# Kernel tuning notes

Measured on AMD Instinct MI355X. Metric: run time of the kernel, lower is better.

The kernel has to match this reference:

```python
import jax, jax.numpy as jnp
import numpy as np

N = 500_000
K = 16
E = N * K
H = 256


def _linear_params(key, fan_in, fan_out):
    k1, k2 = jax.random.split(key)
    bound = 1.0 / np.sqrt(fan_in)
    W = jax.random.uniform(k1, (fan_in, fan_out), jnp.float32, -bound, bound)
    b = jax.random.uniform(k2, (fan_out,), jnp.float32, -bound, bound)
    return W, b


def setup_inputs() -> dict:
    key = jax.random.key(0)
    ks = jax.random.split(key, 10)
    x = jax.random.normal(ks[0], (N, 3), jnp.float32)
    edge_index = jax.random.randint(ks[1], (2, E), 0, N, jnp.int64)
    edge_attr = jax.random.normal(ks[2], (E, 1), jnp.float32)
    W1, b1 = _linear_params(ks[3], K, H)          # GNN1 message MLP: Linear(k, 256)
    We1, be1 = _linear_params(ks[4], H, 128)      # encoder Linear(256,128)
    We2, be2 = _linear_params(ks[5], 128, 6)      # encoder Linear(128,6)
    Wd1, bd1 = _linear_params(ks[6], 6, 128)      # decoder Linear(6,128)
    Wd2, bd2 = _linear_params(ks[7], 128, H)      # decoder Linear(128,256)
    Wo, bo = _linear_params(ks[8], H, 1)          # output Linear(256,1)
    return {"x": x, "edge_index": edge_index, "edge_attr": edge_attr,
            "W1": W1, "b1": b1, "We1": We1, "be1": be1, "We2": We2, "be2": be2,
            "Wd1": Wd1, "bd1": bd1, "Wd2": Wd2, "bd2": bd2, "Wo": Wo, "bo": bo}


def reference(x, edge_index, edge_attr, W1, b1, We1, be1, We2, be2,
              Wd1, bd1, Wd2, bd2, Wo, bo):
    # GNN1: messages are edge_attr verbatim (x_i/x_j ignored); aggregate reshapes
    # all E scalar messages into (N, k) (k edges per node, contiguous) and runs
    # Linear(k,256)+Tanh. Note: LSTM and GCN4 branches in the torch code are dead
    # (GNN1 ignores its node-feature input), so they do not affect the output.
    k = W1.shape[0]
    msgs = edge_attr.reshape(-1, k)                    # (N, k)
    h = jnp.tanh(msgs @ W1 + b1)                       # (N, 256)
    # second L1 call produces the identical result (depends only on edge_attr)
    z = jnp.tanh(jnp.tanh(h @ We1 + be1) @ We2 + be2)  # encoder -> (N, 6)
    d = jnp.tanh(z @ Wd1 + bd1) @ Wd2 + bd2            # decoder -> (N, 256)
    out = jax.nn.sigmoid(jnp.tanh(d) @ Wo + bo)        # (N, 1)
    return out[:, 0]                                   # squeeze(dim=1) -> (N,)
```

## Files before the change

kernel.cpp:

```cpp
#include <hip/hip_runtime.h>


#define N_NODES 500000

#define OFF_W1 0
#define OFF_W2 8192
#define OFF_W3 73728
#define OFF_W4 77824
#define OFF_W5 86016
#define OFF_WO 151552
#define OFF_B1 152576
#define OFF_B2 153600
#define OFF_B3 154112
#define OFF_B4 154176
#define OFF_B5 154688
#define OFF_EXTRA 155712
#define OFF_ZERO  155728
#define IMG_END   156240
#define IMG_ALLOC 156672

#define LDS_SZ IMG_ALLOC

#define SCONST (-2.8853900817779268f)

typedef _Float16 half8  __attribute__((ext_vector_type(8)));
typedef __fp16   pk16x2 __attribute__((ext_vector_type(2)));
typedef float    f32x4  __attribute__((ext_vector_type(4)));
typedef int      int4v  __attribute__((ext_vector_type(4)));

__device__ __align__(16) char g_img[IMG_ALLOC];

static __device__ __forceinline__ unsigned pack_f16_rne(float a, float b) {
  _Float16 ha = (_Float16)a, hb = (_Float16)b;
  unsigned short ua = __builtin_bit_cast(unsigned short, ha);
  unsigned short ub = __builtin_bit_cast(unsigned short, hb);
  return (unsigned)ua | ((unsigned)ub << 16);
}
static __device__ __forceinline__ int pkrtz(float a, float b) {
  pk16x2 h = __builtin_amdgcn_cvt_pkrtz(a, b);
  return __builtin_bit_cast(int, h);
}
static __device__ __forceinline__ float sig2(float y) {
  float e = __builtin_amdgcn_exp2f(y);
  return __builtin_amdgcn_rcpf(1.0f + e);
}
static __device__ __forceinline__ float sigmoid_f(float x) {
  float e = __builtin_amdgcn_exp2f(x * -1.4426950408889634f);
  return __builtin_amdgcn_rcpf(1.0f + e);
}
static __device__ __forceinline__ f32x4 mfma16(half8 a, int4v b, f32x4 c) {
  return __builtin_amdgcn_mfma_f32_16x16x32_f16(a, __builtin_bit_cast(half8, b), c, 0, 0, 0);
}
static __device__ __forceinline__ half8 lda(const char* smem, int off) {
  return *(const half8*)(smem + off);
}
static __device__ __forceinline__ f32x4 ldf4(const char* smem, int off) {
  return *(const f32x4*)(smem + off);
}
#define FENCE() __builtin_amdgcn_sched_barrier(0)

struct PK2 { int lo, hi; };
static __device__ __forceinline__ PK2 tp(f32x4 a) {
  PK2 p;
  p.lo = pkrtz(sig2(a.x), sig2(a.y));
  p.hi = pkrtz(sig2(a.z), sig2(a.w));
  return p;
}

__global__ __launch_bounds__(256)
void gnn_prep(const float* __restrict__ W1,  const float* __restrict__ b1,
              const float* __restrict__ We1, const float* __restrict__ be1,
              const float* __restrict__ We2, const float* __restrict__ be2,
              const float* __restrict__ Wd1, const float* __restrict__ bd1,
              const float* __restrict__ Wd2, const float* __restrict__ bd2,
              const float* __restrict__ Wo,  const float* __restrict__ bo)
{
  __shared__ float sb[832];
  const int tid = threadIdx.x;
  const int bx = blockIdx.x;

  if (bx >= 153) {
    float* gB2 = (float*)(g_img + OFF_B2);
    float* gB3 = (float*)(g_img + OFF_B3);
    float* gB4 = (float*)(g_img + OFF_B4);
    float* gB5 = (float*)(g_img + OFF_B5);
    if (bx == 153) {
      int col = tid & 127, part = tid >> 7;
      float s = 0.0f;
      for (int r = 0; r < 128; ++r) s += We1[(part * 128 + r) * 128 + col];
      sb[tid] = s;
      __syncthreads();
      if (tid < 128) gB2[tid] = SCONST * (be1[tid] - (sb[tid] + sb[128 + tid]));
    } else if (bx == 154) {
      float s = 0.0f;
      for (int r = 0; r < 128; ++r) s += Wd2[r * 256 + tid];
      gB5[tid] = SCONST * (bd2[tid] - s);
    } else {
      for (int j = tid; j < 768; j += 256) sb[j] = We2[j];
      if (tid >= 192) {
        int i = tid - 192;
        sb[768 + i] = Wo[4 * i] + Wo[4 * i + 1] + Wo[4 * i + 2] + Wo[4 * i + 3];
      }
      __syncthreads();
      if (tid < 6) {
        float s = 0.0f;
        for (int k = 0; k < 128; ++k) s += sb[k * 6 + tid];
        gB3[tid] = SCONST * (be2[tid] - s);
      } else if (tid < 16) {
        gB3[tid] = 0.0f;
      } else if (tid == 16) {
        float s = 0.0f;
        for (int i = 0; i < 64; ++i) s += sb[768 + i];
        *(float*)(g_img + OFF_EXTRA) = bo[0] - s;
      } else if (tid >= 32 && tid < 160) {
        int i = tid - 32;
        float s = 0.0f;
        for (int k = 0; k < 6; ++k) s += Wd1[k * 128 + i];
        gB4[i] = SCONST * (bd1[i] - s);
      }
    }
    return;
  }

  int off = (bx * 256 + tid) * 4;
  if (off >= IMG_END) return;
  if (off >= OFF_B2 && off < OFF_EXTRA + 4) return;
  unsigned val;
  if (off < OFF_W2) {
    int rel = off;
    int mi = rel >> 9, li = (rel >> 4) & 31, j2 = (rel >> 2) & 3;
    int fout = mi * 16 + (li & 15);
    int k0 = (li >> 4) * 8 + j2 * 2;
    val = pack_f16_rne(SCONST * W1[k0 * 256 + fout], SCONST * W1[(k0 + 1) * 256 + fout]);
  } else if (off < OFF_W3) {
    int rel = off - OFF_W2;
    int blk = rel >> 10, li = (rel >> 4) & 63, j2 = (rel >> 2) & 3;
    int mi = blk >> 3, ki = blk & 7;
    int fout = mi * 16 + (li & 15);
    int k0 = ki * 32 + 4 * (li >> 4) + 16 * (j2 >> 1) + 2 * (j2 & 1);
    val = pack_f16_rne(2.0f * SCONST * We1[k0 * 128 + fout],
                       2.0f * SCONST * We1[(k0 + 1) * 128 + fout]);
  } else if (off < OFF_W4) {
    int rel = off - OFF_W3;
    int ki = rel >> 10, li = (rel >> 4) & 63, j2 = (rel >> 2) & 3;
    int fo = li & 15;
    int k0 = ki * 32 + 4 * (li >> 4) + 16 * (j2 >> 1) + 2 * (j2 & 1);
    float a = (fo < 6) ? 2.0f * SCONST * We2[k0 * 6 + fo] : 0.0f;
    float b = (fo < 6) ? 2.0f * SCONST * We2[(k0 + 1) * 6 + fo] : 0.0f;
    val = pack_f16_rne(a, b);
  } else if (off < OFF_W5) {
    int rel = off - OFF_W4;
    int mi = rel >> 10, li = (rel >> 4) & 63, j2 = (rel >> 2) & 3;
    int fout = mi * 16 + (li & 15);
    int qa = li >> 4;
    unsigned v = 0;
    if (j2 < 2) {
      int k0 = 4 * qa + 2 * j2;
      float a = (k0 < 6)     ? 2.0f * SCONST * Wd1[k0 * 128 + fout]       : 0.0f;
      float b = (k0 + 1 < 6) ? 2.0f * SCONST * Wd1[(k0 + 1) * 128 + fout] : 0.0f;
      v = pack_f16_rne(a, b);
    }
    val = v;
  } else if (off < OFF_WO) {
    int rel = off - OFF_W5;
    int blk = rel >> 10, li = (rel >> 4) & 63, j2 = (rel >> 2) & 3;
    int mi = blk >> 2, ki = blk & 3;
    int fout = mi * 16 + (li & 15);
    int k0 = ki * 32 + 4 * (li >> 4) + 16 * (j2 >> 1) + 2 * (j2 & 1);
    val = pack_f16_rne(2.0f * SCONST * Wd2[k0 * 256 + fout],
                       2.0f * SCONST * Wd2[(k0 + 1) * 256 + fout]);
  } else if (off < OFF_B1) {
    val = __builtin_bit_cast(unsigned, 2.0f * Wo[(off - OFF_WO) >> 2]);
  } else if (off < OFF_B2) {
    val = __builtin_bit_cast(unsigned, SCONST * b1[(off - OFF_B1) >> 2]);
  } else {
    val = 0;
  }
  *(unsigned*)(g_img + off) = val;
}

static __device__ __forceinline__ void stage_chunk(const char* src, char* dst) {
  __builtin_amdgcn_global_load_lds(
      (const __attribute__((address_space(1))) void*)src,
      (__attribute__((address_space(3))) void*)dst, 16, 0, 0);
}

#define L1_PAIR(KO, OUT_G0, OUT_G1) do {                                   \
    half8 Ae = lda(smem, w1b + (2*(KO))*w1s);                              \
    half8 Ao = lda(smem, w1b + (2*(KO)+1)*w1s);                            \
    f32x4 be_ = ldf4(smem, OFF_B1 + (2*(KO))*64 + q*16);                   \
    f32x4 bo_ = ldf4(smem, OFF_B1 + (2*(KO)+1)*64 + q*16);                 \
    f32x4 ae0 = mfma16(Ae, b1g0, be_);                                     \
    f32x4 ae1 = mfma16(Ae, b1g1, be_);                                     \
    f32x4 ao0 = mfma16(Ao, b1g0, bo_);                                     \
    f32x4 ao1 = mfma16(Ao, b1g1, bo_);                                     \
    PK2 pe0 = tp(ae0), po0 = tp(ao0), pe1 = tp(ae1), po1 = tp(ao1);        \
    OUT_G0.x = pe0.lo; OUT_G0.y = pe0.hi; OUT_G0.z = po0.lo; OUT_G0.w = po0.hi; \
    OUT_G1.x = pe1.lo; OUT_G1.y = pe1.hi; OUT_G1.z = po1.lo; OUT_G1.w = po1.hi; \
    FENCE();                                                               \
  } while (0)

#define L2_MI(MI, ACC0, ACC1) do {                                                            \
    f32x4 bb = ldf4(smem, OFF_B2 + (MI)*64 + q*16);                                           \
    ACC0 = bb; ACC1 = bb;                                                                     \
    half8 A;                                                                                  \
    A = lda(smem, OFF_W2 + ((MI)*8+0)*1024 + ln*16); ACC0 = mfma16(A, c2g0_0, ACC0); ACC1 = mfma16(A, c2g1_0, ACC1); \
    A = lda(smem, OFF_W2 + ((MI)*8+1)*1024 + ln*16); ACC0 = mfma16(A, c2g0_1, ACC0); ACC1 = mfma16(A, c2g1_1, ACC1); \
    A = lda(smem, OFF_W2 + ((MI)*8+2)*1024 + ln*16); ACC0 = mfma16(A, c2g0_2, ACC0); ACC1 = mfma16(A, c2g1_2, ACC1); \
    A = lda(smem, OFF_W2 + ((MI)*8+3)*1024 + ln*16); ACC0 = mfma16(A, c2g0_3, ACC0); ACC1 = mfma16(A, c2g1_3, ACC1); \
    A = lda(smem, OFF_W2 + ((MI)*8+4)*1024 + ln*16); ACC0 = mfma16(A, c2g0_4, ACC0); ACC1 = mfma16(A, c2g1_4, ACC1); \
    A = lda(smem, OFF_W2 + ((MI)*8+5)*1024 + ln*16); ACC0 = mfma16(A, c2g0_5, ACC0); ACC1 = mfma16(A, c2g1_5, ACC1); \
    A = lda(smem, OFF_W2 + ((MI)*8+6)*1024 + ln*16); ACC0 = mfma16(A, c2g0_6, ACC0); ACC1 = mfma16(A, c2g1_6, ACC1); \
    A = lda(smem, OFF_W2 + ((MI)*8+7)*1024 + ln*16); ACC0 = mfma16(A, c2g0_7, ACC0); ACC1 = mfma16(A, c2g1_7, ACC1); \
  } while (0)

#define L2_PAIR(KO, OUT_G0, OUT_G1) do {                                   \
    f32x4 ve0, ve1, vo0, vo1;                                              \
    L2_MI(2*(KO),   ve0, ve1);                                             \
    FENCE();                                                               \
    L2_MI(2*(KO)+1, vo0, vo1);                                             \
    PK2 pe0 = tp(ve0), po0 = tp(vo0), pe1 = tp(ve1), po1 = tp(vo1);        \
    OUT_G0.x = pe0.lo; OUT_G0.y = pe0.hi; OUT_G0.z = po0.lo; OUT_G0.w = po0.hi; \
    OUT_G1.x = pe1.lo; OUT_G1.y = pe1.hi; OUT_G1.z = po1.lo; OUT_G1.w = po1.hi; \
    FENCE();                                                               \
  } while (0)

#define L4_MI(MI, ACC0, ACC1) do {                                         \
    f32x4 bb = ldf4(smem, OFF_B4 + (MI)*64 + q*16);                        \
    half8 A = lda(smem, OFF_W4 + (MI)*1024 + ln*16);                       \
    ACC0 = mfma16(A, b4g0, bb);                                            \
    ACC1 = mfma16(A, b4g1, bb);                                            \
  } while (0)

#define L4_PAIR(KO, OUT_G0, OUT_G1) do {                                   \
    f32x4 ve0, ve1, vo0, vo1;                                              \
    L4_MI(2*(KO),   ve0, ve1);                                             \
    L4_MI(2*(KO)+1, vo0, vo1);                                             \
    PK2 pe0 = tp(ve0), po0 = tp(vo0), pe1 = tp(ve1), po1 = tp(vo1);        \
    OUT_G0.x = pe0.lo; OUT_G0.y = pe0.hi; OUT_G0.z = po0.lo; OUT_G0.w = po0.hi; \
    OUT_G1.x = pe1.lo; OUT_G1.y = pe1.hi; OUT_G1.z = po1.lo; OUT_G1.w = po1.hi; \
  } while (0)

#define L5_MI(MI) do {                                                                        \
    f32x4 bb = ldf4(smem, OFF_B5 + (MI)*64 + q*16);                                           \
    f32x4 a0 = bb, a1 = bb;                                                                   \
    half8 A;                                                                                  \
    A = lda(smem, OFF_W5 + ((MI)*4+0)*1024 + ln*16); a0 = mfma16(A, c5g0_0, a0); a1 = mfma16(A, c5g1_0, a1); \
    A = lda(smem, OFF_W5 + ((MI)*4+1)*1024 + ln*16); a0 = mfma16(A, c5g0_1, a0); a1 = mfma16(A, c5g1_1, a1); \
    A = lda(smem, OFF_W5 + ((MI)*4+2)*1024 + ln*16); a0 = mfma16(A, c5g0_2, a0); a1 = mfma16(A, c5g1_2, a1); \
    A = lda(smem, OFF_W5 + ((MI)*4+3)*1024 + ln*16); a0 = mfma16(A, c5g0_3, a0); a1 = mfma16(A, c5g1_3, a1); \
    f32x4 wo = ldf4(smem, OFF_WO + (MI)*64 + q*16);                                           \
    part0 += sig2(a0.x)*wo.x + sig2(a0.y)*wo.y + sig2(a0.z)*wo.z + sig2(a0.w)*wo.w;           \
    part1 += sig2(a1.x)*wo.x + sig2(a1.y)*wo.y + sig2(a1.z)*wo.z + sig2(a1.w)*wo.w;           \
  } while (0)

__global__ __launch_bounds__(512)
void gnn_fused(const float* __restrict__ ea, float* __restrict__ out)
{
  __shared__ __align__(16) char smem[LDS_SZ];
  const int tid = threadIdx.x;
  const int wv = tid >> 6, ln = tid & 63;

#pragma unroll 1
  for (int r = 0; r < 20; ++r) {
    int cb = (r * 8 + wv) << 6;
    if (cb < 9765) {
      stage_chunk(g_img + (size_t)cb * 16 + ln * 16,
                  smem + (size_t)cb * 16 + ln * 16);
    }
  }
  __syncthreads();

  const int q = ln >> 4, c = ln & 15;
  const bool qlo = (q < 2);
  const int lnl16 = (ln & 31) * 16;
  const int w1b = qlo ? (OFF_W1 + lnl16) : (OFF_ZERO + lnl16);
  const int w1s = qlo ? 512 : 0;
  const float bo2 = *(const float*)(smem + OFF_EXTRA);

  const int NG = N_NODES / 32;
  const int g0i = blockIdx.x * 8 + wv;
  const int gstep = gridDim.x << 3;
#pragma unroll 1
  for (int g = g0i; g < NG; g += gstep) {
    const int base = g * 32;

    int nl = base + (q >> 1) * 16 + c;
    const f32x4* ea4 = (const f32x4*)ea;
    size_t eb = (size_t)nl * 4 + (size_t)((q & 1) * 2);
    f32x4 vlo = ea4[eb];
    f32x4 vhi = ea4[eb + 1];
    int4v b1g0;
    b1g0.x = pkrtz(vlo.x, vlo.y); b1g0.y = pkrtz(vlo.z, vlo.w);
    b1g0.z = pkrtz(vhi.x, vhi.y); b1g0.w = pkrtz(vhi.z, vhi.w);
    int sh = (ln + 32) & 63;
    int4v b1g1;
    b1g1.x = __shfl(b1g0.x, sh, 64); b1g1.y = __shfl(b1g0.y, sh, 64);
    b1g1.z = __shfl(b1g0.z, sh, 64); b1g1.w = __shfl(b1g0.w, sh, 64);

    int4v c2g0_0, c2g0_1, c2g0_2, c2g0_3, c2g0_4, c2g0_5, c2g0_6, c2g0_7;
    int4v c2g1_0, c2g1_1, c2g1_2, c2g1_3, c2g1_4, c2g1_5, c2g1_6, c2g1_7;
    L1_PAIR(0, c2g0_0, c2g1_0);
    L1_PAIR(1, c2g0_1, c2g1_1);
    L1_PAIR(2, c2g0_2, c2g1_2);
    L1_PAIR(3, c2g0_3, c2g1_3);
    L1_PAIR(4, c2g0_4, c2g1_4);
    L1_PAIR(5, c2g0_5, c2g1_5);
    L1_PAIR(6, c2g0_6, c2g1_6);
    L1_PAIR(7, c2g0_7, c2g1_7);

    int4v c3g0_0, c3g0_1, c3g0_2, c3g0_3;
    int4v c3g1_0, c3g1_1, c3g1_2, c3g1_3;
    L2_PAIR(0, c3g0_0, c3g1_0);
    L2_PAIR(1, c3g0_1, c3g1_1);
    L2_PAIR(2, c3g0_2, c3g1_2);
    L2_PAIR(3, c3g0_3, c3g1_3);

    f32x4 bb3 = ldf4(smem, OFF_B3 + q * 16);
    f32x4 z0 = bb3, z1 = bb3;
    half8 A;
    A = lda(smem, OFF_W3 + 0 * 1024 + ln * 16); z0 = mfma16(A, c3g0_0, z0); z1 = mfma16(A, c3g1_0, z1);
    A = lda(smem, OFF_W3 + 1 * 1024 + ln * 16); z0 = mfma16(A, c3g0_1, z0); z1 = mfma16(A, c3g1_1, z1);
    A = lda(smem, OFF_W3 + 2 * 1024 + ln * 16); z0 = mfma16(A, c3g0_2, z0); z1 = mfma16(A, c3g1_2, z1);
    A = lda(smem, OFF_W3 + 3 * 1024 + ln * 16); z0 = mfma16(A, c3g0_3, z0); z1 = mfma16(A, c3g1_3, z1);
    PK2 p3g0 = tp(z0);
    PK2 p3g1 = tp(z1);
    FENCE();

    int4v b4g0, b4g1;
    b4g0.x = p3g0.lo; b4g0.y = p3g0.hi; b4g0.z = 0; b4g0.w = 0;
    b4g1.x = p3g1.lo; b4g1.y = p3g1.hi; b4g1.z = 0; b4g1.w = 0;

    int4v c5g0_0, c5g0_1, c5g0_2, c5g0_3;
    int4v c5g1_0, c5g1_1, c5g1_2, c5g1_3;
    L4_PAIR(0, c5g0_0, c5g1_0);
    L4_PAIR(1, c5g0_1, c5g1_1);
    L4_PAIR(2, c5g0_2, c5g1_2);
    L4_PAIR(3, c5g0_3, c5g1_3);

    float part0 = 0.0f, part1 = 0.0f;
    L5_MI(0);  L5_MI(1);  L5_MI(2);  L5_MI(3);
    L5_MI(4);  L5_MI(5);  L5_MI(6);  L5_MI(7);
    L5_MI(8);  L5_MI(9);  L5_MI(10); L5_MI(11);
    L5_MI(12); L5_MI(13); L5_MI(14); L5_MI(15);

    part0 += __shfl_xor(part0, 16, 64); part0 += __shfl_xor(part0, 32, 64);
    part1 += __shfl_xor(part1, 16, 64); part1 += __shfl_xor(part1, 32, 64);
    if (q < 2) {
      int node = base + q * 16 + c;
      float v = ((q == 0) ? part0 : part1) + bo2;
      out[node] = sigmoid_f(v);
    }
  }
}

extern "C" void kernel_launch(void* const* d_in, const int* in_sizes, int n_in,
                              void* d_out, int out_size, void* d_ws, size_t ws_size,
                              hipStream_t stream) {
  (void)in_sizes; (void)n_in; (void)ws_size; (void)out_size; (void)d_ws;
  const float* ea  = (const float*)d_in[2];
  const float* W1  = (const float*)d_in[3];
  const float* b1  = (const float*)d_in[4];
  const float* We1 = (const float*)d_in[5];
  const float* be1 = (const float*)d_in[6];
  const float* We2 = (const float*)d_in[7];
  const float* be2 = (const float*)d_in[8];
  const float* Wd1 = (const float*)d_in[9];
  const float* bd1 = (const float*)d_in[10];
  const float* Wd2 = (const float*)d_in[11];
  const float* bd2 = (const float*)d_in[12];
  const float* Wo  = (const float*)d_in[13];
  const float* bo  = (const float*)d_in[14];

  gnn_prep<<<dim3(156), dim3(256), 0, stream>>>(
      W1, b1, We1, be1, We2, be2, Wd1, bd1, Wd2, bd2, Wo, bo);
  gnn_fused<<<dim3(256), dim3(512), 0, stream>>>(ea, (float*)d_out);
}
```

Measured before the change: 233.3 us.

## Interleave layer-1 activation production with layer-2 MFMA accumulation

Rather than computing all 16 layer-1 activation fragments first and then running layer 2, each layer-1 k-chunk now feeds layer 2 straight away, adding into 16 persistent fp32 accumulators initialised from the bias. This replaces 16 live packed layer-1 fragments with 16 live f32x4 accumulators and removes the FENCE points between the stages. The aim is to let the MFMA pipe overlap the tanh/pack work of the next chunk. The trade-off is higher accumulator register pressure, which could lower occupancy or cause spills.

Result: no change. 236.0 us (median of 2 runs) (+1.1%).

```diff
diff --git a/kernel.cpp b/kernel.cpp
--- a/kernel.cpp
+++ b/kernel.cpp
@@ -185,7 +185,7 @@
       (__attribute__((address_space(3))) void*)dst, 16, 0, 0);
 }
 
-#define L1_PAIR(KO, OUT_G0, OUT_G1) do {                                   \
+#define L12_STEP(KO) do {                                                  \
     half8 Ae = lda(smem, w1b + (2*(KO))*w1s);                              \
     half8 Ao = lda(smem, w1b + (2*(KO)+1)*w1s);                            \
     f32x4 be_ = ldf4(smem, OFF_B1 + (2*(KO))*64 + q*16);                   \
@@ -195,34 +195,24 @@
     f32x4 ao0 = mfma16(Ao, b1g0, bo_);                                     \
     f32x4 ao1 = mfma16(Ao, b1g1, bo_);                                     \
     PK2 pe0 = tp(ae0), po0 = tp(ao0), pe1 = tp(ae1), po1 = tp(ao1);        \
+    int4v c0, c1;                                                          \
+    c0.x = pe0.lo; c0.y = pe0.hi; c0.z = po0.lo; c0.w = po0.hi;            \
+    c1.x = pe1.lo; c1.y = pe1.hi; c1.z = po1.lo; c1.w = po1.hi;            \
+    half8 A;                                                               \
+    A = lda(smem, OFF_W2 + (0*8+(KO))*1024 + ln*16); a2g0_0 = mfma16(A, c0, a2g0_0); a2g1_0 = mfma16(A, c1, a2g1_0); \
+    A = lda(smem, OFF_W2 + (1*8+(KO))*1024 + ln*16); a2g0_1 = mfma16(A, c0, a2g0_1); a2g1_1 = mfma16(A, c1, a2g1_1); \
+    A = lda(smem, OFF_W2 + (2*8+(KO))*1024 + ln*16); a2g0_2 = mfma16(A, c0, a2g0_2); a2g1_2 = mfma16(A, c1, a2g1_2); \
+    A = lda(smem, OFF_W2 + (3*8+(KO))*1024 + ln*16); a2g0_3 = mfma16(A, c0, a2g0_3); a2g1_3 = mfma16(A, c1, a2g1_3); \
+    A = lda(smem, OFF_W2 + (4*8+(KO))*1024 + ln*16); a2g0_4 = mfma16(A, c0, a2g0_4); a2g1_4 = mfma16(A, c1, a2g1_4); \
+    A = lda(smem, OFF_W2 + (5*8+(KO))*1024 + ln*16); a2g0_5 = mfma16(A, c0, a2g0_5); a2g1_5 = mfma16(A, c1, a2g1_5); \
+    A = lda(smem, OFF_W2 + (6*8+(KO))*1024 + ln*16); a2g0_6 = mfma16(A, c0, a2g0_6); a2g1_6 = mfma16(A, c1, a2g1_6); \
+    A = lda(smem, OFF_W2 + (7*8+(KO))*1024 + ln*16); a2g0_7 = mfma16(A, c0, a2g0_7); a2g1_7 = mfma16(A, c1, a2g1_7); \
+  } while (0)
+
+#define L2_FIN(J, OUT_G0, OUT_G1, AE0, AO0, AE1, AO1) do {                 \
+    PK2 pe0 = tp(AE0), po0 = tp(AO0), pe1 = tp(AE1), po1 = tp(AO1);        \
     OUT_G0.x = pe0.lo; OUT_G0.y = pe0.hi; OUT_G0.z = po0.lo; OUT_G0.w = po0.hi; \
     OUT_G1.x = pe1.lo; OUT_G1.y = pe1.hi; OUT_G1.z = po1.lo; OUT_G1.w = po1.hi; \
-    FENCE();                                                               \
-  } while (0)
-
-#define L2_MI(MI, ACC0, ACC1) do {                                                            \
-    f32x4 bb = ldf4(smem, OFF_B2 + (MI)*64 + q*16);                                           \
-    ACC0 = bb; ACC1 = bb;                                                                     \
-    half8 A;                                                                                  \
-    A = lda(smem, OFF_W2 + ((MI)*8+0)*1024 + ln*16); ACC0 = mfma16(A, c2g0_0, ACC0); ACC1 = mfma16(A, c2g1_0, ACC1); \
-    A = lda(smem, OFF_W2 + ((MI)*8+1)*1024 + ln*16); ACC0 = mfma16(A, c2g0_1, ACC0); ACC1 = mfma16(A, c2g1_1, ACC1); \
-    A = lda(smem, OFF_W2 + ((MI)*8+2)*1024 + ln*16); ACC0 = mfma16(A, c2g0_2, ACC0); ACC1 = mfma16(A, c2g1_2, ACC1); \
-    A = lda(smem, OFF_W2 + ((MI)*8+3)*1024 + ln*16); ACC0 = mfma16(A, c2g0_3, ACC0); ACC1 = mfma16(A, c2g1_3, ACC1); \
-    A = lda(smem, OFF_W2 + ((MI)*8+4)*1024 + ln*16); ACC0 = mfma16(A, c2g0_4, ACC0); ACC1 = mfma16(A, c2g1_4, ACC1); \
-    A = lda(smem, OFF_W2 + ((MI)*8+5)*1024 + ln*16); ACC0 = mfma16(A, c2g0_5, ACC0); ACC1 = mfma16(A, c2g1_5, ACC1); \
-    A = lda(smem, OFF_W2 + ((MI)*8+6)*1024 + ln*16); ACC0 = mfma16(A, c2g0_6, ACC0); ACC1 = mfma16(A, c2g1_6, ACC1); \
-    A = lda(smem, OFF_W2 + ((MI)*8+7)*1024 + ln*16); ACC0 = mfma16(A, c2g0_7, ACC0); ACC1 = mfma16(A, c2g1_7, ACC1); \
-  } while (0)
-
-#define L2_PAIR(KO, OUT_G0, OUT_G1) do {                                   \
-    f32x4 ve0, ve1, vo0, vo1;                                              \
-    L2_MI(2*(KO),   ve0, ve1);                                             \
-    FENCE();                                                               \
-    L2_MI(2*(KO)+1, vo0, vo1);                                             \
-    PK2 pe0 = tp(ve0), po0 = tp(vo0), pe1 = tp(ve1), po1 = tp(vo1);        \
-    OUT_G0.x = pe0.lo; OUT_G0.y = pe0.hi; OUT_G0.z = po0.lo; OUT_G0.w = po0.hi; \
-    OUT_G1.x = pe1.lo; OUT_G1.y = pe1.hi; OUT_G1.z = po1.lo; OUT_G1.w = po1.hi; \
-    FENCE();                                                               \
   } while (0)
 
 #define L4_MI(MI, ACC0, ACC1) do {                                         \
@@ -298,23 +288,31 @@
     b1g1.x = __shfl(b1g0.x, sh, 64); b1g1.y = __shfl(b1g0.y, sh, 64);
     b1g1.z = __shfl(b1g0.z, sh, 64); b1g1.w = __shfl(b1g0.w, sh, 64);
 
-    int4v c2g0_0, c2g0_1, c2g0_2, c2g0_3, c2g0_4, c2g0_5, c2g0_6, c2g0_7;
-    int4v c2g1_0, c2g1_1, c2g1_2, c2g1_3, c2g1_4, c2g1_5, c2g1_6, c2g1_7;
-    L1_PAIR(0, c2g0_0, c2g1_0);
-    L1_PAIR(1, c2g0_1, c2g1_1);
-    L1_PAIR(2, c2g0_2, c2g1_2);
-    L1_PAIR(3, c2g0_3, c2g1_3);
-    L1_PAIR(4, c2g0_4, c2g1_4);
-    L1_PAIR(5, c2g0_5, c2g1_5);
-    L1_PAIR(6, c2g0_6, c2g1_6);
-    L1_PAIR(7, c2g0_7, c2g1_7);
+    f32x4 a2g0_0, a2g0_1, a2g0_2, a2g0_3, a2g0_4, a2g0_5, a2g0_6, a2g0_7;
+    f32x4 a2g1_0, a2g1_1, a2g1_2, a2g1_3, a2g1_4, a2g1_5, a2g1_6, a2g1_7;
+    a2g0_0 = ldf4(smem, OFF_B2 + 0*64 + q*16); a2g1_0 = a2g0_0;
+    a2g0_1 = ldf4(smem, OFF_B2 + 1*64 + q*16); a2g1_1 = a2g0_1;
+    a2g0_2 = ldf4(smem, OFF_B2 + 2*64 + q*16); a2g1_2 = a2g0_2;
+    a2g0_3 = ldf4(smem, OFF_B2 + 3*64 + q*16); a2g1_3 = a2g0_3;
+    a2g0_4 = ldf4(smem, OFF_B2 + 4*64 + q*16); a2g1_4 = a2g0_4;
+    a2g0_5 = ldf4(smem, OFF_B2 + 5*64 + q*16); a2g1_5 = a2g0_5;
+    a2g0_6 = ldf4(smem, OFF_B2 + 6*64 + q*16); a2g1_6 = a2g0_6;
+    a2g0_7 = ldf4(smem, OFF_B2 + 7*64 + q*16); a2g1_7 = a2g0_7;
+    L12_STEP(0);
+    L12_STEP(1);
+    L12_STEP(2);
+    L12_STEP(3);
+    L12_STEP(4);
+    L12_STEP(5);
+    L12_STEP(6);
+    L12_STEP(7);
 
     int4v c3g0_0, c3g0_1, c3g0_2, c3g0_3;
     int4v c3g1_0, c3g1_1, c3g1_2, c3g1_3;
-    L2_PAIR(0, c3g0_0, c3g1_0);
-    L2_PAIR(1, c3g0_1, c3g1_1);
-    L2_PAIR(2, c3g0_2, c3g1_2);
-    L2_PAIR(3, c3g0_3, c3g1_3);
+    L2_FIN(0, c3g0_0, c3g1_0, a2g0_0, a2g0_1, a2g1_0, a2g1_1);
+    L2_FIN(1, c3g0_1, c3g1_1, a2g0_2, a2g0_3, a2g1_2, a2g1_3);
+    L2_FIN(2, c3g0_2, c3g1_2, a2g0_4, a2g0_5, a2g1_4, a2g1_5);
+    L2_FIN(3, c3g0_3, c3g1_3, a2g0_6, a2g0_7, a2g1_6, a2g1_7);
 
     f32x4 bb3 = ldf4(smem, OFF_B3 + q * 16);
     f32x4 z0 = bb3, z1 = bb3;
```

## Split fused MLP kernel into encoder and decoder kernels to halve LDS

Applied to the files above, without the earlier changes.

Splits the single fused kernel into two. The encoder kernel writes the 6-wide latent z as packed fp16 to workspace, and the decoder kernel reads it back. Each kernel now stages only its own weights into LDS, roughly 78 KB and 77 KB instead of about 156 KB. That should allow two blocks per CU, so grids double to 512 blocks. The cost is an extra launch and a round trip of the latent through global memory, about 8 MB each way.

Result: slower. 379.6 us (+62.7%).

```diff
diff --git a/kernel.cpp b/kernel.cpp
--- a/kernel.cpp
+++ b/kernel.cpp
@@ -6,20 +6,27 @@
 #define OFF_W1 0
 #define OFF_W2 8192
 #define OFF_W3 73728
-#define OFF_W4 77824
-#define OFF_W5 86016
-#define OFF_WO 151552
-#define OFF_B1 152576
-#define OFF_B2 153600
-#define OFF_B3 154112
-#define OFF_B4 154176
-#define OFF_B5 154688
-#define OFF_EXTRA 155712
-#define OFF_ZERO  155728
-#define IMG_END   156240
+#define OFF_B1 77824
+#define OFF_B2 78848
+#define OFF_B3 79360
+#define OFF_ZERO 79424
+#define K1_LDS 79872
+#define K2_BASE 79872
+#define OFF_W4 79872
+#define OFF_W5 88064
+#define OFF_WO 153600
+#define OFF_B4 154624
+#define OFF_B5 155136
+#define OFF_EXTRA 156160
+#define IMG_END 156176
+#define K2_LDS 76800
 #define IMG_ALLOC 156672
-
-#define LDS_SZ IMG_ALLOC
+#define SM_W4   0
+#define SM_W5   8192
+#define SM_WO   73728
+#define SM_B4   74752
+#define SM_B5   75264
+#define SM_EXTRA 76288
 
 #define SCONST (-2.8853900817779268f)
 
@@ -124,7 +131,8 @@
 
   int off = (bx * 256 + tid) * 4;
   if (off >= IMG_END) return;
-  if (off >= OFF_B2 && off < OFF_EXTRA + 4) return;
+  if ((off >= OFF_B2 && off < OFF_ZERO) ||
+      (off >= OFF_B4 && off < OFF_EXTRA + 4)) return;
   unsigned val;
   if (off < OFF_W2) {
     int rel = off;
@@ -140,7 +148,7 @@
     int k0 = ki * 32 + 4 * (li >> 4) + 16 * (j2 >> 1) + 2 * (j2 & 1);
     val = pack_f16_rne(2.0f * SCONST * We1[k0 * 128 + fout],
                        2.0f * SCONST * We1[(k0 + 1) * 128 + fout]);
-  } else if (off < OFF_W4) {
+  } else if (off < OFF_B1) {
     int rel = off - OFF_W3;
     int ki = rel >> 10, li = (rel >> 4) & 63, j2 = (rel >> 2) & 3;
     int fo = li & 15;
@@ -148,6 +156,10 @@
     float a = (fo < 6) ? 2.0f * SCONST * We2[k0 * 6 + fo] : 0.0f;
     float b = (fo < 6) ? 2.0f * SCONST * We2[(k0 + 1) * 6 + fo] : 0.0f;
     val = pack_f16_rne(a, b);
+  } else if (off < OFF_B2) {
+    val = __builtin_bit_cast(unsigned, SCONST * b1[(off - OFF_B1) >> 2]);
+  } else if (off < OFF_W4) {
+    val = 0;
   } else if (off < OFF_W5) {
     int rel = off - OFF_W4;
     int mi = rel >> 10, li = (rel >> 4) & 63, j2 = (rel >> 2) & 3;
@@ -169,10 +181,8 @@
     int k0 = ki * 32 + 4 * (li >> 4) + 16 * (j2 >> 1) + 2 * (j2 & 1);
     val = pack_f16_rne(2.0f * SCONST * Wd2[k0 * 256 + fout],
                        2.0f * SCONST * Wd2[(k0 + 1) * 256 + fout]);
-  } else if (off < OFF_B1) {
+  } else if (off < OFF_B4) {
     val = __builtin_bit_cast(unsigned, 2.0f * Wo[(off - OFF_WO) >> 2]);
-  } else if (off < OFF_B2) {
-    val = __builtin_bit_cast(unsigned, SCONST * b1[(off - OFF_B1) >> 2]);
   } else {
     val = 0;
   }
@@ -225,46 +235,17 @@
     FENCE();                                                               \
   } while (0)
 
-#define L4_MI(MI, ACC0, ACC1) do {                                         \
-    f32x4 bb = ldf4(smem, OFF_B4 + (MI)*64 + q*16);                        \
-    half8 A = lda(smem, OFF_W4 + (MI)*1024 + ln*16);                       \
-    ACC0 = mfma16(A, b4g0, bb);                                            \
-    ACC1 = mfma16(A, b4g1, bb);                                            \
-  } while (0)
-
-#define L4_PAIR(KO, OUT_G0, OUT_G1) do {                                   \
-    f32x4 ve0, ve1, vo0, vo1;                                              \
-    L4_MI(2*(KO),   ve0, ve1);                                             \
-    L4_MI(2*(KO)+1, vo0, vo1);                                             \
-    PK2 pe0 = tp(ve0), po0 = tp(vo0), pe1 = tp(ve1), po1 = tp(vo1);        \
-    OUT_G0.x = pe0.lo; OUT_G0.y = pe0.hi; OUT_G0.z = po0.lo; OUT_G0.w = po0.hi; \
-    OUT_G1.x = pe1.lo; OUT_G1.y = pe1.hi; OUT_G1.z = po1.lo; OUT_G1.w = po1.hi; \
-  } while (0)
-
-#define L5_MI(MI) do {                                                                        \
-    f32x4 bb = ldf4(smem, OFF_B5 + (MI)*64 + q*16);                                           \
-    f32x4 a0 = bb, a1 = bb;                                                                   \
-    half8 A;                                                                                  \
-    A = lda(smem, OFF_W5 + ((MI)*4+0)*1024 + ln*16); a0 = mfma16(A, c5g0_0, a0); a1 = mfma16(A, c5g1_0, a1); \
-    A = lda(smem, OFF_W5 + ((MI)*4+1)*1024 + ln*16); a0 = mfma16(A, c5g0_1, a0); a1 = mfma16(A, c5g1_1, a1); \
-    A = lda(smem, OFF_W5 + ((MI)*4+2)*1024 + ln*16); a0 = mfma16(A, c5g0_2, a0); a1 = mfma16(A, c5g1_2, a1); \
-    A = lda(smem, OFF_W5 + ((MI)*4+3)*1024 + ln*16); a0 = mfma16(A, c5g0_3, a0); a1 = mfma16(A, c5g1_3, a1); \
-    f32x4 wo = ldf4(smem, OFF_WO + (MI)*64 + q*16);                                           \
-    part0 += sig2(a0.x)*wo.x + sig2(a0.y)*wo.y + sig2(a0.z)*wo.z + sig2(a0.w)*wo.w;           \
-    part1 += sig2(a1.x)*wo.x + sig2(a1.y)*wo.y + sig2(a1.z)*wo.z + sig2(a1.w)*wo.w;           \
-  } while (0)
-
 __global__ __launch_bounds__(512)
-void gnn_fused(const float* __restrict__ ea, float* __restrict__ out)
+void gnn_k1(const float* __restrict__ ea, int4v* __restrict__ zbuf)
 {
-  __shared__ __align__(16) char smem[LDS_SZ];
+  __shared__ __align__(16) char smem[K1_LDS];
   const int tid = threadIdx.x;
   const int wv = tid >> 6, ln = tid & 63;
 
 #pragma unroll 1
-  for (int r = 0; r < 20; ++r) {
+  for (int r = 0; r < 10; ++r) {
     int cb = (r * 8 + wv) << 6;
-    if (cb < 9765) {
+    if (cb < K1_LDS / 16) {
       stage_chunk(g_img + (size_t)cb * 16 + ln * 16,
                   smem + (size_t)cb * 16 + ln * 16);
     }
@@ -274,9 +255,8 @@
   const int q = ln >> 4, c = ln & 15;
   const bool qlo = (q < 2);
   const int lnl16 = (ln & 31) * 16;
-  const int w1b = qlo ? (OFF_W1 + lnl16) : (OFF_ZERO + lnl16);
+  const int w1b = qlo ? (OFF_W1 + lnl16) : OFF_ZERO;
   const int w1s = qlo ? 512 : 0;
-  const float bo2 = *(const float*)(smem + OFF_EXTRA);
 
   const int NG = N_NODES / 32;
   const int g0i = blockIdx.x * 8 + wv;
@@ -325,11 +305,77 @@
     A = lda(smem, OFF_W3 + 3 * 1024 + ln * 16); z0 = mfma16(A, c3g0_3, z0); z1 = mfma16(A, c3g1_3, z1);
     PK2 p3g0 = tp(z0);
     PK2 p3g1 = tp(z1);
-    FENCE();
+
+    if (ln < 32) {
+      int4v zv;
+      zv.x = p3g0.lo; zv.y = p3g0.hi; zv.z = p3g1.lo; zv.w = p3g1.hi;
+      zbuf[(size_t)g * 32 + ln] = zv;
+    }
+  }
+}
+
+#define L4_MI(MI, ACC0, ACC1) do {                                         \
+    f32x4 bb = ldf4(smem, SM_B4 + (MI)*64 + q*16);                         \
+    half8 A = lda(smem, SM_W4 + (MI)*1024 + ln*16);                        \
+    ACC0 = mfma16(A, b4g0, bb);                                            \
+    ACC1 = mfma16(A, b4g1, bb);                                            \
+  } while (0)
+
+#define L4_PAIR(KO, OUT_G0, OUT_G1) do {                                   \
+    f32x4 ve0, ve1, vo0, vo1;                                              \
+    L4_MI(2*(KO),   ve0, ve1);                                             \
+    L4_MI(2*(KO)+1, vo0, vo1);                                             \
+    PK2 pe0 = tp(ve0), po0 = tp(vo0), pe1 = tp(ve1), po1 = tp(vo1);        \
+    OUT_G0.x = pe0.lo; OUT_G0.y = pe0.hi; OUT_G0.z = po0.lo; OUT_G0.w = po0.hi; \
+    OUT_G1.x = pe1.lo; OUT_G1.y = pe1.hi; OUT_G1.z = po1.lo; OUT_G1.w = po1.hi; \
+  } while (0)
+
+#define L5_MI(MI) do {                                                                        \
+    f32x4 bb = ldf4(smem, SM_B5 + (MI)*64 + q*16);                                            \
+    f32x4 a0 = bb, a1 = bb;                                                                   \
+    half8 A;                                                                                  \
+    A = lda(smem, SM_W5 + ((MI)*4+0)*1024 + ln*16); a0 = mfma16(A, c5g0_0, a0); a1 = mfma16(A, c5g1_0, a1); \
+    A = lda(smem, SM_W5 + ((MI)*4+1)*1024 + ln*16); a0 = mfma16(A, c5g0_1, a0); a1 = mfma16(A, c5g1_1, a1); \
+    A = lda(smem, SM_W5 + ((MI)*4+2)*1024 + ln*16); a0 = mfma16(A, c5g0_2, a0); a1 = mfma16(A, c5g1_2, a1); \
+    A = lda(smem, SM_W5 + ((MI)*4+3)*1024 + ln*16); a0 = mfma16(A, c5g0_3, a0); a1 = mfma16(A, c5g1_3, a1); \
+    f32x4 wo = ldf4(smem, SM_WO + (MI)*64 + q*16);                                            \
+    part0 += sig2(a0.x)*wo.x + sig2(a0.y)*wo.y + sig2(a0.z)*wo.z + sig2(a0.w)*wo.w;           \
+    part1 += sig2(a1.x)*wo.x + sig2(a1.y)*wo.y + sig2(a1.z)*wo.z + sig2(a1.w)*wo.w;           \
+  } while (0)
+
+__global__ __launch_bounds__(512)
+void gnn_k2(const int4v* __restrict__ zbuf, float* __restrict__ out)
+{
+  __shared__ __align__(16) char smem[K2_LDS];
+  const int tid = threadIdx.x;
+  const int wv = tid >> 6, ln = tid & 63;
+
+#pragma unroll 1
+  for (int r = 0; r < 10; ++r) {
+    int cb = (r * 8 + wv) << 6;
+    if (cb < K2_LDS / 16) {
+      stage_chunk(g_img + K2_BASE + (size_t)cb * 16 + ln * 16,
+                  smem + (size_t)cb * 16 + ln * 16);
+    }
+  }
+  __syncthreads();
+
+  const int q = ln >> 4, c = ln & 15;
+  const float bo2 = *(const float*)(smem + SM_EXTRA);
+
+  const int NG = N_NODES / 32;
+  const int g0i = blockIdx.x * 8 + wv;
+  const int gstep = gridDim.x << 3;
+#pragma unroll 1
+  for (int g = g0i; g < NG; g += gstep) {
+    const int base = g * 32;
+
+    int4v zv = {0, 0, 0, 0};
+    if (ln < 32) zv = zbuf[(size_t)g * 32 + ln];
 
     int4v b4g0, b4g1;
-    b4g0.x = p3g0.lo; b4g0.y = p3g0.hi; b4g0.z = 0; b4g0.w = 0;
-    b4g1.x = p3g1.lo; b4g1.y = p3g1.hi; b4g1.z = 0; b4g1.w = 0;
+    b4g0.x = zv.x; b4g0.y = zv.y; b4g0.z = 0; b4g0.w = 0;
+    b4g1.x = zv.z; b4g1.y = zv.w; b4g1.z = 0; b4g1.w = 0;
 
     int4v c5g0_0, c5g0_1, c5g0_2, c5g0_3;
     int4v c5g1_0, c5g1_1, c5g1_2, c5g1_3;
@@ -357,7 +403,7 @@
 extern "C" void kernel_launch(void* const* d_in, const int* in_sizes, int n_in,
                               void* d_out, int out_size, void* d_ws, size_t ws_size,
                               hipStream_t stream) {
-  (void)in_sizes; (void)n_in; (void)ws_size; (void)out_size; (void)d_ws;
+  (void)in_sizes; (void)n_in; (void)ws_size; (void)out_size;
   const float* ea  = (const float*)d_in[2];
   const float* W1  = (const float*)d_in[3];
   const float* b1  = (const float*)d_in[4];
@@ -374,5 +420,6 @@
 
   gnn_prep<<<dim3(156), dim3(256), 0, stream>>>(
       W1, b1, We1, be1, We2, be2, Wd1, bd1, Wd2, bd2, Wo, bo);
-  gnn_fused<<<dim3(256), dim3(512), 0, stream>>>(ea, (float*)d_out);
-}
+  gnn_k1<<<dim3(512), dim3(512), 0, stream>>>(ea, (int4v*)d_ws);
+  gnn_k2<<<dim3(512), dim3(512), 0, stream>>>((const int4v*)d_ws, (float*)d_out);
+}
```
